# Kernel optimization log

Hardware: AMD Instinct MI355X
Metric: run time of the kernel (lower is better)

## Reference

```python
import jax, jax.numpy as jnp
import numpy as np
from math import sqrt

B, H, S, D = 4, 16, 8192, 64
M = 64  # num_samples (<= D since ortho_features=True)
SCALE = 0.1  # keep exp() numerically sane for randn inputs


def _gram_schmidt(mat):
    # unnormalized Gram-Schmidt over columns, matching the torch module
    d, m = mat.shape
    out = np.zeros_like(mat)
    out[:, 0] = mat[:, 0]
    for i in range(1, m):
        v = mat[:, i]
        U = out[:, :i]                      # [d, i]
        coef = (U.T @ v) / np.sum(U * U, axis=0)
        out[:, i] = v - U @ coef
    return out


def setup_inputs() -> dict:
    key = jax.random.key(0)
    kq, kk, kv = jax.random.split(key, 3)
    query = jax.random.normal(kq, (B, H, S, D), dtype=jnp.float32) * SCALE
    key_t = jax.random.normal(kk, (B, H, S, D), dtype=jnp.float32) * SCALE
    value = jax.random.normal(kv, (B, H, S, D), dtype=jnp.float32) * SCALE
    rng = np.random.default_rng(0)
    omega = jnp.asarray(_gram_schmidt(rng.standard_normal((D, M)).astype(np.float32)))
    return {"query": query, "key": key_t, "value": value, "omega": omega}


def _pos_features(x, omega, m):
    # 1/sqrt(m) * exp(-||x||^2/2) * exp(x @ omega)   -> [..., S, m]
    h = jnp.exp(-0.5 * jnp.sum(x * x, axis=-1)) * (1.0 / sqrt(m))  # [B,H,S]
    return h[..., None] * jnp.exp(jnp.einsum('bhsd,dm->bhsm', x, omega))


def reference(query, key, value, omega):
    d = query.shape[-1]
    m = omega.shape[-1]
    q_prime = _pos_features(query, omega, m)   # [B,H,S,m]
    k_prime = _pos_features(key, omega, m)     # [B,H,S,m]
    ones = jnp.ones(value.shape[:-1] + (1,), dtype=value.dtype)
    C = jnp.concatenate([value, ones], axis=-1)               # [B,H,S,d+1]
    buf1 = jnp.einsum('bhsm,bhsc->bhmc', k_prime, C)          # [B,H,m,d+1]
    buf2 = jnp.einsum('bhsm,bhmc->bhsc', q_prime, buf1)       # [B,H,S,d+1]
    num = buf2[..., :d]                                       # [B,H,S,d]
    den = buf2[..., d:]                                       # [B,H,S,1]
    return num / den
```

## Files before the change

### kernel.cpp

```cpp
#include <hip/hip_runtime.h>

typedef short short8 __attribute__((ext_vector_type(8)));
typedef float f32x4 __attribute__((ext_vector_type(4)));

namespace {
constexpr int Sc = 8192, Dc = 64;
constexpr int NH = 64;
constexpr int CH = 1024;
constexpr int TPT = CH / 64;
constexpr int NCHUNK = Sc / CH;
constexpr size_t DEN_OFF = (size_t)NH * 4096;
constexpr size_t WT_OFF_BYTES = (DEN_OFF + NH * 64) * 4;
}

__device__ __forceinline__ unsigned bf16rtne(float x) {
  unsigned u = __builtin_bit_cast(unsigned, x);
  return (u + 0x7fffu + ((u >> 16) & 1u)) >> 16;
}
__device__ __forceinline__ unsigned pkhl(float x) {
  unsigned u = __builtin_bit_cast(unsigned, x);
  unsigned rh = (u + 0x7fffu + ((u >> 16) & 1u)) & 0xffff0000u;
  float res = x - __builtin_bit_cast(float, rh);
  return (rh >> 16) | (__builtin_bit_cast(unsigned, res) & 0xffff0000u);
}
__device__ __forceinline__ void bsplit(float x, short& hi, short& lo) {
  unsigned p = pkhl(x);
  hi = (short)(p & 0xffff);
  lo = (short)(p >> 16);
}
__device__ __forceinline__ short8 exhi(uint4 q0, uint4 q1) {
  union { unsigned u[4]; short8 s; } r;
  r.u[0] = __builtin_amdgcn_perm(q0.y, q0.x, 0x05040100u);
  r.u[1] = __builtin_amdgcn_perm(q0.w, q0.z, 0x05040100u);
  r.u[2] = __builtin_amdgcn_perm(q1.y, q1.x, 0x05040100u);
  r.u[3] = __builtin_amdgcn_perm(q1.w, q1.z, 0x05040100u);
  return r.s;
}
__device__ __forceinline__ short8 exlo(uint4 q0, uint4 q1) {
  union { unsigned u[4]; short8 s; } r;
  r.u[0] = __builtin_amdgcn_perm(q0.y, q0.x, 0x07060302u);
  r.u[1] = __builtin_amdgcn_perm(q0.w, q0.z, 0x07060302u);
  r.u[2] = __builtin_amdgcn_perm(q1.y, q1.x, 0x07060302u);
  r.u[3] = __builtin_amdgcn_perm(q1.w, q1.z, 0x07060302u);
  return r.s;
}

__global__ void p0(const float* __restrict__ omega, short* __restrict__ wT) {
  int i = blockIdx.x * 256 + threadIdx.x;
  if (i < 4096) {
    int m = i >> 6, d = i & 63;
    short hi, lo;
    bsplit(omega[d * 64 + m], hi, lo);
    wT[m * 64 + d] = hi;
    wT[4096 + m * 64 + d] = lo;
  }
}

__global__ __launch_bounds__(256, 2) void p1(
    const float* __restrict__ Kg, const float* __restrict__ Vg,
    const short* __restrict__ wT, float* __restrict__ b1, float* __restrict__ den) {
  __shared__ unsigned Kpk[64 * 68];
  __shared__ unsigned VT[64 * 68];
  __shared__ unsigned PT[64 * 68];
  __shared__ float ssq[64];

  const int t = threadIdx.x;
  const int lane = t & 63;
  const int w = t >> 6;
  const int a = lane & 15;
  const int g = lane >> 4;
  const int bh = blockIdx.x / NCHUNK, ch = blockIdx.x % NCHUNK;
  const float* Kb = Kg + ((size_t)bh * Sc + (size_t)ch * CH) * Dc;
  const float* Vb = Vg + ((size_t)bh * Sc + (size_t)ch * CH) * Dc;

  short8 wfh[4][2], wfl[4][2];
#pragma unroll
  for (int mt = 0; mt < 4; ++mt)
#pragma unroll
    for (int ks = 0; ks < 2; ++ks) {
      int off = (a + 16 * mt) * 64 + 32 * ks + 8 * g;
      wfh[mt][ks] = *(const short8*)(wT + off);
      wfl[mt][ks] = *(const short8*)(wT + 4096 + off);
    }

  float4 kreg[4], vreg[4];
  auto load_tile = [&](int tile) {
    const float4* Kt = (const float4*)(Kb + (size_t)tile * 64 * Dc);
    const float4* Vt = (const float4*)(Vb + (size_t)tile * 64 * Dc);
#pragma unroll
    for (int rr = 0; rr < 4; ++rr) {
      kreg[rr] = Kt[rr * 256 + t];
      vreg[rr] = Vt[rr * 256 + t];
    }
  };
  auto store_tile = [&]() {
#pragma unroll
    for (int rr = 0; rr < 4; ++rr) {
      int idx = rr * 256 + t;
      int row = idx >> 4;
      int c4 = idx & 15;
      float4 kv = kreg[rr];
      uint4 kp;
      kp.x = pkhl(kv.x); kp.y = pkhl(kv.y);
      kp.z = pkhl(kv.z); kp.w = pkhl(kv.w);
      *(uint4*)&Kpk[row * 68 + 4 * c4] = kp;
      float ps = kv.x * kv.x + kv.y * kv.y + kv.z * kv.z + kv.w * kv.w;
      ps += __shfl_xor(ps, 1, 64); ps += __shfl_xor(ps, 2, 64);
      ps += __shfl_xor(ps, 4, 64); ps += __shfl_xor(ps, 8, 64);
      if (c4 == 0) ssq[row] = ps;
      float4 vv = vreg[rr];
      int sw = row ^ (4 * ((c4 >> 1) & 7));
      VT[(4 * c4 + 0) * 68 + sw] = bf16rtne(vv.x);
      VT[(4 * c4 + 1) * 68 + sw] = bf16rtne(vv.y);
      VT[(4 * c4 + 2) * 68 + sw] = bf16rtne(vv.z);
      VT[(4 * c4 + 3) * 68 + sw] = bf16rtne(vv.w);
    }
  };

  f32x4 B1a[4];
#pragma unroll
  for (int ct = 0; ct < 4; ++ct) B1a[ct] = (f32x4){0.f, 0.f, 0.f, 0.f};
  float dpart[4] = {0.f, 0.f, 0.f, 0.f};

  load_tile(0);
  store_tile();
  __syncthreads();

  for (int tile = 0; tile < TPT; ++tile) {
    if (tile + 1 < TPT) load_tile(tile + 1);

    f32x4 X[4];
#pragma unroll
    for (int mt = 0; mt < 4; ++mt) X[mt] = (f32x4){0.f, 0.f, 0.f, 0.f};
#pragma unroll
    for (int ks = 0; ks < 2; ++ks) {
      const unsigned* kb = &Kpk[(16 * w + a) * 68 + 32 * ks + 8 * g];
      uint4 q0 = *(const uint4*)kb;
      uint4 q1 = *(const uint4*)(kb + 4);
      short8 ah = exhi(q0, q1), al = exlo(q0, q1);
#pragma unroll
      for (int mt = 0; mt < 4; ++mt) {
        X[mt] = __builtin_amdgcn_mfma_f32_16x16x32_bf16(ah, wfh[mt][ks], X[mt], 0, 0, 0);
        X[mt] = __builtin_amdgcn_mfma_f32_16x16x32_bf16(ah, wfl[mt][ks], X[mt], 0, 0, 0);
        X[mt] = __builtin_amdgcn_mfma_f32_16x16x32_bf16(al, wfh[mt][ks], X[mt], 0, 0, 0);
      }
    }

    float sq[4];
#pragma unroll
    for (int r = 0; r < 4; ++r) sq[r] = ssq[16 * w + 4 * g + r];
#pragma unroll
    for (int mt = 0; mt < 4; ++mt) {
      uint4 pp;
      float p_;
      p_ = 0.125f * __expf(X[mt][0] - 0.5f * sq[0]); dpart[mt] += p_; pp.x = bf16rtne(p_);
      p_ = 0.125f * __expf(X[mt][1] - 0.5f * sq[1]); dpart[mt] += p_; pp.y = bf16rtne(p_);
      p_ = 0.125f * __expf(X[mt][2] - 0.5f * sq[2]); dpart[mt] += p_; pp.z = bf16rtne(p_);
      p_ = 0.125f * __expf(X[mt][3] - 0.5f * sq[3]); dpart[mt] += p_; pp.w = bf16rtne(p_);
      *(uint4*)&PT[(16 * mt + a) * 68 + 16 * w + 4 * g] = pp;
    }
    __syncthreads();

#pragma unroll
    for (int ks = 0; ks < 2; ++ks) {
      const unsigned* pb = &PT[(16 * w + a) * 68 + 32 * ks + 8 * g];
      uint4 r0 = *(const uint4*)pb;
      uint4 r1 = *(const uint4*)(pb + 4);
      short8 pah = exhi(r0, r1);
#pragma unroll
      for (int ct = 0; ct < 4; ++ct) {
        int c = 16 * ct + a;
        int kk4 = 4 * ((2 * ct + (a >> 3)) & 7);
        int s0 = (32 * ks + 8 * g) ^ kk4;
        int s1 = (32 * ks + 8 * g + 4) ^ kk4;
        const unsigned* vb = &VT[c * 68];
        uint4 v0 = *(const uint4*)(vb + s0);
        uint4 v1 = *(const uint4*)(vb + s1);
        short8 vh = exhi(v0, v1);
        B1a[ct] = __builtin_amdgcn_mfma_f32_16x16x32_bf16(pah, vh, B1a[ct], 0, 0, 0);
      }
    }
    __syncthreads();
    if (tile + 1 < TPT) store_tile();
    __syncthreads();
  }

  float* b1h = b1 + (size_t)bh * 4096;
#pragma unroll
  for (int ct = 0; ct < 4; ++ct)
#pragma unroll
    for (int r = 0; r < 4; ++r)
      atomicAdd(&b1h[(16 * w + 4 * g + r) * 64 + 16 * ct + a], B1a[ct][r]);
#pragma unroll
  for (int mt = 0; mt < 4; ++mt) {
    float v = dpart[mt];
    v += __shfl_xor(v, 16, 64);
    v += __shfl_xor(v, 32, 64);
    if (g == 0) atomicAdd(&den[bh * 64 + 16 * mt + a], v);
  }
}

__global__ __launch_bounds__(256, 2) void p2(
    const float* __restrict__ Qg, const short* __restrict__ wT,
    const float* __restrict__ b1, const float* __restrict__ den,
    float* __restrict__ out) {
  __shared__ unsigned Qpk[64 * 68];
  __shared__ unsigned QP[64 * 68];
  __shared__ short B1h[64 * 72], B1l[64 * 72];
  __shared__ float denv[64];
  __shared__ float ssq[64];

  const int t = threadIdx.x;
  const int lane = t & 63;
  const int w = t >> 6;
  const int a = lane & 15;
  const int g = lane >> 4;
  const int bh = blockIdx.x / NCHUNK, ch = blockIdx.x % NCHUNK;
  const float* Qb = Qg + ((size_t)bh * Sc + (size_t)ch * CH) * Dc;

  short8 wfh[4][2], wfl[4][2];
#pragma unroll
  for (int mt = 0; mt < 4; ++mt)
#pragma unroll
    for (int ks = 0; ks < 2; ++ks) {
      int off = (a + 16 * mt) * 64 + 32 * ks + 8 * g;
      wfh[mt][ks] = *(const short8*)(wT + off);
      wfl[mt][ks] = *(const short8*)(wT + 4096 + off);
    }

  const float* b1g = b1 + (size_t)bh * 4096;
  for (int i = t; i < 4096; i += 256) {
    int m = i >> 6, c = i & 63;
    short hi, lo;
    bsplit(b1g[i], hi, lo);
    B1h[c * 72 + m] = hi;
    B1l[c * 72 + m] = lo;
  }
  if (t < 64) denv[t] = den[bh * 64 + t];

  float4 qreg[4];
  auto load_tile = [&](int tile) {
    const float4* Qt = (const float4*)(Qb + (size_t)tile * 64 * Dc);
#pragma unroll
    for (int rr = 0; rr < 4; ++rr) qreg[rr] = Qt[rr * 256 + t];
  };
  auto store_tile = [&]() {
#pragma unroll
    for (int rr = 0; rr < 4; ++rr) {
      int idx = rr * 256 + t;
      int row = idx >> 4;
      int c4 = idx & 15;
      float4 kv = qreg[rr];
      uint4 qp;
      qp.x = pkhl(kv.x); qp.y = pkhl(kv.y);
      qp.z = pkhl(kv.z); qp.w = pkhl(kv.w);
      *(uint4*)&Qpk[row * 68 + 4 * c4] = qp;
      float ps = kv.x * kv.x + kv.y * kv.y + kv.z * kv.z + kv.w * kv.w;
      ps += __shfl_xor(ps, 1, 64); ps += __shfl_xor(ps, 2, 64);
      ps += __shfl_xor(ps, 4, 64); ps += __shfl_xor(ps, 8, 64);
      if (c4 == 0) ssq[row] = ps;
    }
  };

  load_tile(0);
  store_tile();
  __syncthreads();

  for (int tile = 0; tile < TPT; ++tile) {
    if (tile + 1 < TPT) load_tile(tile + 1);

    f32x4 X[4];
#pragma unroll
    for (int mt = 0; mt < 4; ++mt) X[mt] = (f32x4){0.f, 0.f, 0.f, 0.f};
#pragma unroll
    for (int ks = 0; ks < 2; ++ks) {
      const unsigned* qb = &Qpk[(16 * w + a) * 68 + 32 * ks + 8 * g];
      uint4 q0 = *(const uint4*)qb;
      uint4 q1 = *(const uint4*)(qb + 4);
      short8 ah = exhi(q0, q1), al = exlo(q0, q1);
#pragma unroll
      for (int mt = 0; mt < 4; ++mt) {
        X[mt] = __builtin_amdgcn_mfma_f32_16x16x32_bf16(ah, wfh[mt][ks], X[mt], 0, 0, 0);
        X[mt] = __builtin_amdgcn_mfma_f32_16x16x32_bf16(ah, wfl[mt][ks], X[mt], 0, 0, 0);
        X[mt] = __builtin_amdgcn_mfma_f32_16x16x32_bf16(al, wfh[mt][ks], X[mt], 0, 0, 0);
      }
    }

    float sq[4];
#pragma unroll
    for (int r = 0; r < 4; ++r) sq[r] = ssq[16 * w + 4 * g + r];
    float dv[4];
#pragma unroll
    for (int mt = 0; mt < 4; ++mt) dv[mt] = denv[16 * mt + a];
    float dn[4] = {0.f, 0.f, 0.f, 0.f};
#pragma unroll
    for (int mt = 0; mt < 4; ++mt) {
#pragma unroll
      for (int r = 0; r < 4; ++r) {
        float p_ = 0.125f * __expf(X[mt][r] - 0.5f * sq[r]);
        dn[r] = fmaf(p_, dv[mt], dn[r]);
        QP[(16 * w + 4 * g + r) * 68 + 16 * mt + a] = pkhl(p_);
      }
    }
#pragma unroll
    for (int r = 0; r < 4; ++r) {
      dn[r] += __shfl_xor(dn[r], 1, 64);
      dn[r] += __shfl_xor(dn[r], 2, 64);
      dn[r] += __shfl_xor(dn[r], 4, 64);
      dn[r] += __shfl_xor(dn[r], 8, 64);
    }
    __syncthreads();

    f32x4 O[4];
#pragma unroll
    for (int ct = 0; ct < 4; ++ct) O[ct] = (f32x4){0.f, 0.f, 0.f, 0.f};
#pragma unroll
    for (int ks = 0; ks < 2; ++ks) {
      const unsigned* qb = &QP[(16 * w + a) * 68 + 32 * ks + 8 * g];
      uint4 r0 = *(const uint4*)qb;
      uint4 r1 = *(const uint4*)(qb + 4);
      short8 qh = exhi(r0, r1), ql = exlo(r0, r1);
#pragma unroll
      for (int ct = 0; ct < 4; ++ct) {
        short8 bh_ = *(const short8*)&B1h[(16 * ct + a) * 72 + 32 * ks + 8 * g];
        short8 bl_ = *(const short8*)&B1l[(16 * ct + a) * 72 + 32 * ks + 8 * g];
        O[ct] = __builtin_amdgcn_mfma_f32_16x16x32_bf16(qh, bh_, O[ct], 0, 0, 0);
        O[ct] = __builtin_amdgcn_mfma_f32_16x16x32_bf16(qh, bl_, O[ct], 0, 0, 0);
        O[ct] = __builtin_amdgcn_mfma_f32_16x16x32_bf16(ql, bh_, O[ct], 0, 0, 0);
      }
    }

    float inv[4];
#pragma unroll
    for (int r = 0; r < 4; ++r) inv[r] = 1.0f / dn[r];
    float* ob = out + ((size_t)bh * Sc + (size_t)ch * CH + tile * 64 + 16 * w + 4 * g) * 64;
#pragma unroll
    for (int ct = 0; ct < 4; ++ct)
#pragma unroll
      for (int r = 0; r < 4; ++r)
        ob[r * 64 + 16 * ct + a] = O[ct][r] * inv[r];
    __syncthreads();
    if (tile + 1 < TPT) store_tile();
    __syncthreads();
  }
}

extern "C" void kernel_launch(void* const* d_in, const int* in_sizes, int n_in,
                              void* d_out, int out_size, void* d_ws, size_t ws_size,
                              hipStream_t stream) {
  const float* Q = (const float*)d_in[0];
  const float* K = (const float*)d_in[1];
  const float* V = (const float*)d_in[2];
  const float* omega = (const float*)d_in[3];
  float* outp = (float*)d_out;
  float* b1 = (float*)d_ws;
  float* den = b1 + DEN_OFF;
  short* wT = (short*)((char*)d_ws + WT_OFF_BYTES);

  hipMemsetAsync(d_ws, 0, WT_OFF_BYTES, stream);
  p0<<<16, 256, 0, stream>>>(omega, wT);
  p1<<<NH * NCHUNK, 256, 0, stream>>>(K, V, wT, b1, den);
  p2<<<NH * NCHUNK, 256, 0, stream>>>(Q, wT, b1, den, outp);
}
```

Measured before the change: 146.7 us.

## Pack V transpose as bf16 pairs, halve p1 chunk size, raise occupancy

```diff
diff --git a/kernel.cpp b/kernel.cpp
--- a/kernel.cpp
+++ b/kernel.cpp
@@ -2,13 +2,17 @@
 
 typedef short short8 __attribute__((ext_vector_type(8)));
 typedef float f32x4 __attribute__((ext_vector_type(4)));
+typedef unsigned u32x2 __attribute__((ext_vector_type(2)));
 
 namespace {
 constexpr int Sc = 8192, Dc = 64;
 constexpr int NH = 64;
-constexpr int CH = 1024;
-constexpr int TPT = CH / 64;
-constexpr int NCHUNK = Sc / CH;
+constexpr int CH1 = 512;
+constexpr int TPT1 = CH1 / 64;
+constexpr int NCHUNK1 = Sc / CH1;
+constexpr int CH2 = 1024;
+constexpr int TPT2 = CH2 / 64;
+constexpr int NCHUNK2 = Sc / CH2;
 constexpr size_t DEN_OFF = (size_t)NH * 4096;
 constexpr size_t WT_OFF_BYTES = (DEN_OFF + NH * 64) * 4;
 }
@@ -16,6 +20,9 @@
 __device__ __forceinline__ unsigned bf16rtne(float x) {
   unsigned u = __builtin_bit_cast(unsigned, x);
   return (u + 0x7fffu + ((u >> 16) & 1u)) >> 16;
+}
+__device__ __forceinline__ unsigned pk2bf(float x, float y) {
+  return bf16rtne(x) | (bf16rtne(y) << 16);
 }
 __device__ __forceinline__ unsigned pkhl(float x) {
   unsigned u = __builtin_bit_cast(unsigned, x);
@@ -42,6 +49,14 @@
   r.u[1] = __builtin_amdgcn_perm(q0.w, q0.z, 0x07060302u);
   r.u[2] = __builtin_amdgcn_perm(q1.y, q1.x, 0x07060302u);
   r.u[3] = __builtin_amdgcn_perm(q1.w, q1.z, 0x07060302u);
+  return r.s;
+}
+__device__ __forceinline__ short8 exsel(uint4 q0, uint4 q1, unsigned sel) {
+  union { unsigned u[4]; short8 s; } r;
+  r.u[0] = __builtin_amdgcn_perm(q0.y, q0.x, sel);
+  r.u[1] = __builtin_amdgcn_perm(q0.w, q0.z, sel);
+  r.u[2] = __builtin_amdgcn_perm(q1.y, q1.x, sel);
+  r.u[3] = __builtin_amdgcn_perm(q1.w, q1.z, sel);
   return r.s;
 }
 
@@ -56,11 +71,11 @@
   }
 }
 
-__global__ __launch_bounds__(256, 2) void p1(
+__global__ __launch_bounds__(256, 3) void p1(
     const float* __restrict__ Kg, const float* __restrict__ Vg,
     const short* __restrict__ wT, float* __restrict__ b1, float* __restrict__ den) {
   __shared__ unsigned Kpk[64 * 68];
-  __shared__ unsigned VT[64 * 68];
+  __shared__ unsigned VT[32 * 68];
   __shared__ unsigned PT[64 * 68];
   __shared__ float ssq[64];
 
@@ -69,9 +84,10 @@
   const int w = t >> 6;
   const int a = lane & 15;
   const int g = lane >> 4;
-  const int bh = blockIdx.x / NCHUNK, ch = blockIdx.x % NCHUNK;
-  const float* Kb = Kg + ((size_t)bh * Sc + (size_t)ch * CH) * Dc;
-  const float* Vb = Vg + ((size_t)bh * Sc + (size_t)ch * CH) * Dc;
+  const int bh = blockIdx.x / NCHUNK1, ch = blockIdx.x % NCHUNK1;
+  const float* Kb = Kg + ((size_t)bh * Sc + (size_t)ch * CH1) * Dc;
+  const float* Vb = Vg + ((size_t)bh * Sc + (size_t)ch * CH1) * Dc;
+  const unsigned vsel = (a & 1) ? 0x07060302u : 0x05040100u;
 
   short8 wfh[4][2], wfl[4][2];
 #pragma unroll
@@ -110,10 +126,8 @@
       if (c4 == 0) ssq[row] = ps;
       float4 vv = vreg[rr];
       int sw = row ^ (4 * ((c4 >> 1) & 7));
-      VT[(4 * c4 + 0) * 68 + sw] = bf16rtne(vv.x);
-      VT[(4 * c4 + 1) * 68 + sw] = bf16rtne(vv.y);
-      VT[(4 * c4 + 2) * 68 + sw] = bf16rtne(vv.z);
-      VT[(4 * c4 + 3) * 68 + sw] = bf16rtne(vv.w);
+      VT[(2 * c4 + 0) * 68 + sw] = pk2bf(vv.x, vv.y);
+      VT[(2 * c4 + 1) * 68 + sw] = pk2bf(vv.z, vv.w);
     }
   };
 
@@ -126,8 +140,8 @@
   store_tile();
   __syncthreads();
 
-  for (int tile = 0; tile < TPT; ++tile) {
-    if (tile + 1 < TPT) load_tile(tile + 1);
+  for (int tile = 0; tile < TPT1; ++tile) {
+    if (tile + 1 < TPT1) load_tile(tile + 1);
 
     f32x4 X[4];
 #pragma unroll
@@ -169,19 +183,19 @@
       short8 pah = exhi(r0, r1);
 #pragma unroll
       for (int ct = 0; ct < 4; ++ct) {
-        int c = 16 * ct + a;
+        int c2 = 8 * ct + (a >> 1);
         int kk4 = 4 * ((2 * ct + (a >> 3)) & 7);
         int s0 = (32 * ks + 8 * g) ^ kk4;
         int s1 = (32 * ks + 8 * g + 4) ^ kk4;
-        const unsigned* vb = &VT[c * 68];
+        const unsigned* vb = &VT[c2 * 68];
         uint4 v0 = *(const uint4*)(vb + s0);
         uint4 v1 = *(const uint4*)(vb + s1);
-        short8 vh = exhi(v0, v1);
+        short8 vh = exsel(v0, v1, vsel);
         B1a[ct] = __builtin_amdgcn_mfma_f32_16x16x32_bf16(pah, vh, B1a[ct], 0, 0, 0);
       }
     }
     __syncthreads();
-    if (tile + 1 < TPT) store_tile();
+    if (tile + 1 < TPT1) store_tile();
     __syncthreads();
   }
 
@@ -215,8 +229,8 @@
   const int w = t >> 6;
   const int a = lane & 15;
   const int g = lane >> 4;
-  const int bh = blockIdx.x / NCHUNK, ch = blockIdx.x % NCHUNK;
-  const float* Qb = Qg + ((size_t)bh * Sc + (size_t)ch * CH) * Dc;
+  const int bh = blockIdx.x / NCHUNK2, ch = blockIdx.x % NCHUNK2;
+  const float* Qb = Qg + ((size_t)bh * Sc + (size_t)ch * CH2) * Dc;
 
   short8 wfh[4][2], wfl[4][2];
 #pragma unroll
@@ -266,8 +280,8 @@
   store_tile();
   __syncthreads();
 
-  for (int tile = 0; tile < TPT; ++tile) {
-    if (tile + 1 < TPT) load_tile(tile + 1);
+  for (int tile = 0; tile < TPT2; ++tile) {
+    if (tile + 1 < TPT2) load_tile(tile + 1);
 
     f32x4 X[4];
 #pragma unroll
@@ -333,14 +347,14 @@
     float inv[4];
 #pragma unroll
     for (int r = 0; r < 4; ++r) inv[r] = 1.0f / dn[r];
-    float* ob = out + ((size_t)bh * Sc + (size_t)ch * CH + tile * 64 + 16 * w + 4 * g) * 64;
+    float* ob = out + ((size_t)bh * Sc + (size_t)ch * CH2 + tile * 64 + 16 * w + 4 * g) * 64;
 #pragma unroll
     for (int ct = 0; ct < 4; ++ct)
 #pragma unroll
       for (int r = 0; r < 4; ++r)
         ob[r * 64 + 16 * ct + a] = O[ct][r] * inv[r];
     __syncthreads();
-    if (tile + 1 < TPT) store_tile();
+    if (tile + 1 < TPT2) store_tile();
     __syncthreads();
   }
 }
@@ -359,6 +373,6 @@
 
   hipMemsetAsync(d_ws, 0, WT_OFF_BYTES, stream);
   p0<<<16, 256, 0, stream>>>(omega, wT);
-  p1<<<NH * NCHUNK, 256, 0, stream>>>(K, V, wT, b1, den);
-  p2<<<NH * NCHUNK, 256, 0, stream>>>(Q, wT, b1, den, outp);
-}
+  p1<<<NH * NCHUNK1, 256, 0, stream>>>(K, V, wT, b1, den);
+  p2<<<NH * NCHUNK2, 256, 0, stream>>>(Q, wT, b1, den, outp);
+}
```

After: 191.7 us. +30.7%, slower.
